# Performance work log

Hardware: AMD Instinct MI355X
Metric: run time of the kernel (lower is better)

The kernel has to match this reference:

```python
import jax, jax.numpy as jnp
import numpy as np

K_SYNAPSES = 32          # numberOfSynapsesPerSegment
THETA = 16               # segment activation threshold (k/2 of the +/-1 synapses)


def _make_weight(key, n_neurons, prev_size, k):
    """Dense int8-style EISANI weight: exactly k synapses per neuron, values +/-1, rest 0.
    Mirrors _initialise_layer_weights (non-EI, dense, static-connection branch)."""
    k1, k2 = jax.random.split(key)
    scores = jax.random.uniform(k1, (n_neurons, prev_size))
    _, idx = jax.lax.top_k(scores, k)  # k distinct random columns per neuron
    signs = jnp.where(jax.random.bernoulli(k2, 0.5, (n_neurons, k)), 1.0, -1.0)
    w = jnp.zeros((n_neurons, prev_size), jnp.float32)
    return w.at[jnp.arange(n_neurons)[:, None], idx].set(signs)


def setup_inputs() -> dict:
    key = jax.random.key(0)
    ks = jax.random.split(key, 5)
    B, F, H, C, L = 1024, 4096, 4096, 10, 3  # batch, encodedFeatureSize, hidden, classes, hidden layers
    # binary encoded tabular input (continuous-var thermometer/gray encoding -> {0,1})
    x = (jax.random.uniform(ks[0], (B, F)) > 0.5).astype(jnp.float32)
    w0 = _make_weight(ks[1], H, F, K_SYNAPSES)
    w1 = _make_weight(ks[2], H, H, K_SYNAPSES)
    w2 = _make_weight(ks[3], H, H, K_SYNAPSES)
    out_conn = jax.random.normal(ks[4], (L, H, C), jnp.float32) * 0.02
    return {"x": x, "w0": w0, "w1": w1, "w2": w2, "out_conn": out_conn}


def reference(x, w0, w1, w2, out_conn):
    # Hidden pass: signed binary connection matmul + threshold activation per layer.
    a = x  # [B, F] in {0,1}
    acts = []
    for w in (w0, w1, w2):
        z = a @ w.T                                   # [B, H] integer-valued dot of {0,1} with {-1,0,+1}
        a = (z >= THETA).astype(jnp.float32)          # segment fires if enough synapses active
        acts.append(a)
    acts = jnp.stack(acts)                            # [L, B, H]
    # Output layer: every hidden layer projects to the class scores.
    return jnp.einsum('lbh,lhc->bc', acts, out_conn)  # [B, C]
```

## Files before the change

### kernel.cpp

```cpp
#include <hip/hip_runtime.h>
#include <stdint.h>


__global__ __launch_bounds__(256) void pack_kernel(const float* __restrict__ x,
                                                   uint64_t* __restrict__ bits) {
    const int c  = blockIdx.x * 256 + threadIdx.x;
    const int bg = blockIdx.y;
    const float* xp = x + (size_t)bg * 64 * 4096 + c;
    uint64_t acc = 0;
#pragma unroll
    for (int r = 0; r < 64; ++r) {
        const float v = xp[(size_t)r * 4096];
        acc |= (uint64_t)(v > 0.5f) << r;
    }
    bits[(size_t)bg * 4096 + c] = acc;
}

__global__ __launch_bounds__(256) void sparsify_kernel(const float* __restrict__ w0,
                                                       const float* __restrict__ w1,
                                                       const float* __restrict__ w2,
                                                       uint32_t* __restrict__ syn) {
    const int wid   = blockIdx.x * 4 + (threadIdx.x >> 6);
    const int lane  = threadIdx.x & 63;
    const int layer = wid >> 12;
    const int r     = wid & 4095;
    const float* wp = (layer == 0 ? w0 : (layer == 1 ? w1 : w2)) + (size_t)r * 4096;
    uint32_t* srow  = syn + (size_t)wid * 32;
    const uint64_t lt = (1ull << lane) - 1ull;
    uint32_t base = 0;
    for (int it = 0; it < 16; ++it) {
        const int col = it * 256 + lane * 4;
        const float4 v = *(const float4*)(wp + col);
        const uint64_t m0 = __ballot(v.x != 0.0f);
        const uint64_t m1 = __ballot(v.y != 0.0f);
        const uint64_t m2 = __ballot(v.z != 0.0f);
        const uint64_t m3 = __ballot(v.w != 0.0f);
        const uint32_t t0 = (uint32_t)__popcll(m0), t1 = (uint32_t)__popcll(m1);
        const uint32_t t2 = (uint32_t)__popcll(m2), t3 = (uint32_t)__popcll(m3);
        if (v.x != 0.0f) { const uint32_t s = base + (uint32_t)__popcll(m0 & lt);
            if (s < 32u) srow[s] = (uint32_t)col | (v.x < 0.0f ? 0x80000000u : 0u); }
        if (v.y != 0.0f) { const uint32_t s = base + t0 + (uint32_t)__popcll(m1 & lt);
            if (s < 32u) srow[s] = (uint32_t)(col + 1) | (v.y < 0.0f ? 0x80000000u : 0u); }
        if (v.z != 0.0f) { const uint32_t s = base + t0 + t1 + (uint32_t)__popcll(m2 & lt);
            if (s < 32u) srow[s] = (uint32_t)(col + 2) | (v.z < 0.0f ? 0x80000000u : 0u); }
        if (v.w != 0.0f) { const uint32_t s = base + t0 + t1 + t2 + (uint32_t)__popcll(m3 & lt);
            if (s < 32u) srow[s] = (uint32_t)(col + 3) | (v.w < 0.0f ? 0x80000000u : 0u); }
        base += t0 + t1 + t2 + t3;
    }
}

__global__ __launch_bounds__(256) void layer_kernel(const uint64_t* __restrict__ in_bits,
                                                    const uint32_t* __restrict__ syn,
                                                    uint64_t* __restrict__ out_bits) {
    __shared__ uint64_t lb[4096];
    const int tid = threadIdx.x;
    const int bg  = blockIdx.y;
    const uint64_t* src = in_bits + (size_t)bg * 4096;
#pragma unroll
    for (int i = 0; i < 8; ++i)
        ((uint4*)lb)[i * 256 + tid] = ((const uint4*)src)[i * 256 + tid];
    __syncthreads();

    const int h = blockIdx.x * 256 + tid;
    const uint32_t* srow = syn + (size_t)h * 32;
    uint32_t sw[32];
#pragma unroll
    for (int k = 0; k < 8; ++k)
        *(uint4*)(sw + k * 4) = *(const uint4*)(srow + k * 4);

    uint32_t thr = 16;
#pragma unroll
    for (int k = 0; k < 32; ++k) thr += sw[k] >> 31;

    uint64_t a0 = 0, a1 = 0, a2 = 0, a3 = 0, a4 = 0;
    uint64_t b0 = 0, b1 = 0, b2 = 0, b3 = 0, b4 = 0;
#pragma unroll
    for (int k = 0; k < 32; k += 2) {
        {
            const uint32_t s = sw[k];
            uint64_t c = lb[s & 4095] ^ (uint64_t)(int64_t)((int32_t)s >> 31);
            uint64_t t;
            t = a0 & c; a0 ^= c; c = t;
            t = a1 & c; a1 ^= c; c = t;
            t = a2 & c; a2 ^= c; c = t;
            t = a3 & c; a3 ^= c; c = t;
            a4 ^= c;
        }
        {
            const uint32_t s = sw[k + 1];
            uint64_t c = lb[s & 4095] ^ (uint64_t)(int64_t)((int32_t)s >> 31);
            uint64_t t;
            t = b0 & c; b0 ^= c; c = t;
            t = b1 & c; b1 ^= c; c = t;
            t = b2 & c; b2 ^= c; c = t;
            t = b3 & c; b3 ^= c; c = t;
            b4 ^= c;
        }
    }
    uint64_t c;
    const uint64_t v0 = a0 ^ b0;     c = a0 & b0;
    const uint64_t v1 = a1 ^ b1 ^ c; c = (a1 & b1) | (c & (a1 ^ b1));
    const uint64_t v2 = a2 ^ b2 ^ c; c = (a2 & b2) | (c & (a2 ^ b2));
    const uint64_t v3 = a3 ^ b3 ^ c; c = (a3 & b3) | (c & (a3 ^ b3));
    const uint64_t v4 = a4 ^ b4 ^ c; c = (a4 & b4) | (c & (a4 ^ b4));
    const uint64_t v5 = c;
    uint64_t gt = 0, eq = ~0ull;
    {
        uint64_t tb;
        tb = ((thr >> 5) & 1u) ? ~0ull : 0ull; gt |= eq & v5 & ~tb; eq &= ~(v5 ^ tb);
        tb = ((thr >> 4) & 1u) ? ~0ull : 0ull; gt |= eq & v4 & ~tb; eq &= ~(v4 ^ tb);
        tb = ((thr >> 3) & 1u) ? ~0ull : 0ull; gt |= eq & v3 & ~tb; eq &= ~(v3 ^ tb);
        tb = ((thr >> 2) & 1u) ? ~0ull : 0ull; gt |= eq & v2 & ~tb; eq &= ~(v2 ^ tb);
        tb = ((thr >> 1) & 1u) ? ~0ull : 0ull; gt |= eq & v1 & ~tb; eq &= ~(v1 ^ tb);
        tb = ((thr >> 0) & 1u) ? ~0ull : 0ull; gt |= eq & v0 & ~tb; eq &= ~(v0 ^ tb);
    }
    out_bits[(size_t)bg * 4096 + h] = gt | eq;
}

__global__ __launch_bounds__(256) void out_kernel(const uint64_t* __restrict__ bits,
                                                  const float* __restrict__ oc,
                                                  float* __restrict__ out) {
    __shared__ float red[4][10];
    const int b   = blockIdx.x;
    const int tid = threadIdx.x;
    const int bg  = b >> 6;
    const int sh  = b & 63;
    float acc[10];
#pragma unroll
    for (int cc = 0; cc < 10; ++cc) acc[cc] = 0.0f;
#pragma unroll
    for (int l = 0; l < 3; ++l) {
        const uint64_t* base = bits + (size_t)l * 65536 + (size_t)bg * 4096;
        const float* ocl = oc + (size_t)l * 40960;
#pragma unroll
        for (int i = 0; i < 16; ++i) {
            const int h = i * 256 + tid;
            const uint64_t w = base[h];
            if ((w >> sh) & 1ull) {
                const float* o = ocl + (size_t)h * 10;
#pragma unroll
                for (int cc = 0; cc < 10; ++cc) acc[cc] += o[cc];
            }
        }
    }
#pragma unroll
    for (int cc = 0; cc < 10; ++cc) {
#pragma unroll
        for (int off = 32; off > 0; off >>= 1) acc[cc] += __shfl_down(acc[cc], off);
    }
    const int wave = tid >> 6;
    if ((tid & 63) == 0) {
#pragma unroll
        for (int cc = 0; cc < 10; ++cc) red[wave][cc] = acc[cc];
    }
    __syncthreads();
    if (tid < 10)
        out[(size_t)b * 10 + tid] = red[0][tid] + red[1][tid] + red[2][tid] + red[3][tid];
}

extern "C" void kernel_launch(void* const* d_in, const int* in_sizes, int n_in,
                              void* d_out, int out_size, void* d_ws, size_t ws_size,
                              hipStream_t stream) {
    const float* x  = (const float*)d_in[0];
    const float* w0 = (const float*)d_in[1];
    const float* w1 = (const float*)d_in[2];
    const float* w2 = (const float*)d_in[3];
    const float* oc = (const float*)d_in[4];
    float* out = (float*)d_out;

    uint32_t* syn   = (uint32_t*)d_ws;
    uint64_t* bitsx = (uint64_t*)((char*)d_ws + 2097152);
    uint64_t* bits0 = bitsx + 65536;
    uint64_t* bits1 = bits0 + 65536;
    uint64_t* bits2 = bits1 + 65536;

    pack_kernel<<<dim3(16, 16), 256, 0, stream>>>(x, bitsx);
    sparsify_kernel<<<3072, 256, 0, stream>>>(w0, w1, w2, syn);

    layer_kernel<<<dim3(16, 16), 256, 0, stream>>>(bitsx, syn,          bits0);
    layer_kernel<<<dim3(16, 16), 256, 0, stream>>>(bits0, syn + 131072, bits1);
    layer_kernel<<<dim3(16, 16), 256, 0, stream>>>(bits1, syn + 262144, bits2);

    out_kernel<<<1024, 256, 0, stream>>>(bits0, oc, out);
}
```

Baseline: 237.0 us.

## Fuse layer and output kernels into one cooperative grid-synced kernel

Merges input packing and weight sparsification into a single prep launch, and batches eight float4 weight loads per wave before the ballot compaction. The three layer passes and the output projection become one cooperative kernel of 256 blocks that calls grid.sync between layers. This removes several launch boundaries and inter-kernel gaps. In exchange, the output stage runs on fewer blocks, and the code now depends on every block being co-resident for the grid barrier.

```diff
diff --git a/kernel.cpp b/kernel.cpp
--- a/kernel.cpp
+++ b/kernel.cpp
@@ -1,161 +1,184 @@
 #include <hip/hip_runtime.h>
+#include <hip/hip_cooperative_groups.h>
 #include <stdint.h>
 
-
-__global__ __launch_bounds__(256) void pack_kernel(const float* __restrict__ x,
+namespace cg = cooperative_groups;
+
+
+__global__ __launch_bounds__(256) void prep_kernel(const float* __restrict__ x,
+                                                   const float* __restrict__ w0,
+                                                   const float* __restrict__ w1,
+                                                   const float* __restrict__ w2,
+                                                   uint32_t* __restrict__ syn,
                                                    uint64_t* __restrict__ bits) {
-    const int c  = blockIdx.x * 256 + threadIdx.x;
-    const int bg = blockIdx.y;
-    const float* xp = x + (size_t)bg * 64 * 4096 + c;
-    uint64_t acc = 0;
-#pragma unroll
-    for (int r = 0; r < 64; ++r) {
-        const float v = xp[(size_t)r * 4096];
-        acc |= (uint64_t)(v > 0.5f) << r;
-    }
-    bits[(size_t)bg * 4096 + c] = acc;
-}
-
-__global__ __launch_bounds__(256) void sparsify_kernel(const float* __restrict__ w0,
-                                                       const float* __restrict__ w1,
-                                                       const float* __restrict__ w2,
-                                                       uint32_t* __restrict__ syn) {
-    const int wid   = blockIdx.x * 4 + (threadIdx.x >> 6);
-    const int lane  = threadIdx.x & 63;
-    const int layer = wid >> 12;
-    const int r     = wid & 4095;
-    const float* wp = (layer == 0 ? w0 : (layer == 1 ? w1 : w2)) + (size_t)r * 4096;
-    uint32_t* srow  = syn + (size_t)wid * 32;
-    const uint64_t lt = (1ull << lane) - 1ull;
-    uint32_t base = 0;
-    for (int it = 0; it < 16; ++it) {
-        const int col = it * 256 + lane * 4;
-        const float4 v = *(const float4*)(wp + col);
-        const uint64_t m0 = __ballot(v.x != 0.0f);
-        const uint64_t m1 = __ballot(v.y != 0.0f);
-        const uint64_t m2 = __ballot(v.z != 0.0f);
-        const uint64_t m3 = __ballot(v.w != 0.0f);
-        const uint32_t t0 = (uint32_t)__popcll(m0), t1 = (uint32_t)__popcll(m1);
-        const uint32_t t2 = (uint32_t)__popcll(m2), t3 = (uint32_t)__popcll(m3);
-        if (v.x != 0.0f) { const uint32_t s = base + (uint32_t)__popcll(m0 & lt);
-            if (s < 32u) srow[s] = (uint32_t)col | (v.x < 0.0f ? 0x80000000u : 0u); }
-        if (v.y != 0.0f) { const uint32_t s = base + t0 + (uint32_t)__popcll(m1 & lt);
-            if (s < 32u) srow[s] = (uint32_t)(col + 1) | (v.y < 0.0f ? 0x80000000u : 0u); }
-        if (v.z != 0.0f) { const uint32_t s = base + t0 + t1 + (uint32_t)__popcll(m2 & lt);
-            if (s < 32u) srow[s] = (uint32_t)(col + 2) | (v.z < 0.0f ? 0x80000000u : 0u); }
-        if (v.w != 0.0f) { const uint32_t s = base + t0 + t1 + t2 + (uint32_t)__popcll(m3 & lt);
-            if (s < 32u) srow[s] = (uint32_t)(col + 3) | (v.w < 0.0f ? 0x80000000u : 0u); }
-        base += t0 + t1 + t2 + t3;
+    const int blk = blockIdx.x;
+    const int tid = threadIdx.x;
+    if (blk < 3072) {
+        const int wid   = blk * 4 + (tid >> 6);
+        const int lane  = tid & 63;
+        const int layer = wid >> 12;
+        const int r     = wid & 4095;
+        const float* wp = (layer == 0 ? w0 : (layer == 1 ? w1 : w2)) + (size_t)r * 4096;
+        const float4* wp4 = (const float4*)wp;
+        uint32_t* srow  = syn + (size_t)wid * 32;
+        const uint64_t lt = (1ull << lane) - 1ull;
+        uint32_t base = 0;
+#pragma unroll
+        for (int half = 0; half < 2; ++half) {
+            float4 v[8];
+#pragma unroll
+            for (int it = 0; it < 8; ++it)
+                v[it] = wp4[half * 512 + it * 64 + lane];
+#pragma unroll
+            for (int it = 0; it < 8; ++it) {
+                const int col = half * 2048 + it * 256 + lane * 4;
+                const float4 q = v[it];
+                const uint64_t m0 = __ballot(q.x != 0.0f);
+                const uint64_t m1 = __ballot(q.y != 0.0f);
+                const uint64_t m2 = __ballot(q.z != 0.0f);
+                const uint64_t m3 = __ballot(q.w != 0.0f);
+                const uint32_t t0 = (uint32_t)__popcll(m0), t1 = (uint32_t)__popcll(m1);
+                const uint32_t t2 = (uint32_t)__popcll(m2), t3 = (uint32_t)__popcll(m3);
+                if (q.x != 0.0f) { const uint32_t s = base + (uint32_t)__popcll(m0 & lt);
+                    if (s < 32u) srow[s] = (uint32_t)col | (q.x < 0.0f ? 0x80000000u : 0u); }
+                if (q.y != 0.0f) { const uint32_t s = base + t0 + (uint32_t)__popcll(m1 & lt);
+                    if (s < 32u) srow[s] = (uint32_t)(col + 1) | (q.y < 0.0f ? 0x80000000u : 0u); }
+                if (q.z != 0.0f) { const uint32_t s = base + t0 + t1 + (uint32_t)__popcll(m2 & lt);
+                    if (s < 32u) srow[s] = (uint32_t)(col + 2) | (q.z < 0.0f ? 0x80000000u : 0u); }
+                if (q.w != 0.0f) { const uint32_t s = base + t0 + t1 + t2 + (uint32_t)__popcll(m3 & lt);
+                    if (s < 32u) srow[s] = (uint32_t)(col + 3) | (q.w < 0.0f ? 0x80000000u : 0u); }
+                base += t0 + t1 + t2 + t3;
+            }
+        }
+    } else {
+        const int blk2 = blk - 3072;
+        const int bg   = blk2 >> 4;
+        const int c    = (blk2 & 15) * 256 + tid;
+        const float* xp = x + (size_t)bg * 64 * 4096 + c;
+        uint64_t acc = 0;
+#pragma unroll
+        for (int rr = 0; rr < 64; ++rr) {
+            const float v = xp[(size_t)rr * 4096];
+            acc |= (uint64_t)(v > 0.5f) << rr;
+        }
+        bits[(size_t)bg * 4096 + c] = acc;
     }
 }
 
-__global__ __launch_bounds__(256) void layer_kernel(const uint64_t* __restrict__ in_bits,
-                                                    const uint32_t* __restrict__ syn,
-                                                    uint64_t* __restrict__ out_bits) {
-    __shared__ uint64_t lb[4096];
-    const int tid = threadIdx.x;
-    const int bg  = blockIdx.y;
-    const uint64_t* src = in_bits + (size_t)bg * 4096;
-#pragma unroll
-    for (int i = 0; i < 8; ++i)
-        ((uint4*)lb)[i * 256 + tid] = ((const uint4*)src)[i * 256 + tid];
-    __syncthreads();
-
-    const int h = blockIdx.x * 256 + tid;
-    const uint32_t* srow = syn + (size_t)h * 32;
-    uint32_t sw[32];
-#pragma unroll
-    for (int k = 0; k < 8; ++k)
-        *(uint4*)(sw + k * 4) = *(const uint4*)(srow + k * 4);
-
-    uint32_t thr = 16;
-#pragma unroll
-    for (int k = 0; k < 32; ++k) thr += sw[k] >> 31;
-
-    uint64_t a0 = 0, a1 = 0, a2 = 0, a3 = 0, a4 = 0;
-    uint64_t b0 = 0, b1 = 0, b2 = 0, b3 = 0, b4 = 0;
-#pragma unroll
-    for (int k = 0; k < 32; k += 2) {
-        {
-            const uint32_t s = sw[k];
-            uint64_t c = lb[s & 4095] ^ (uint64_t)(int64_t)((int32_t)s >> 31);
-            uint64_t t;
-            t = a0 & c; a0 ^= c; c = t;
-            t = a1 & c; a1 ^= c; c = t;
-            t = a2 & c; a2 ^= c; c = t;
-            t = a3 & c; a3 ^= c; c = t;
-            a4 ^= c;
-        }
-        {
-            const uint32_t s = sw[k + 1];
-            uint64_t c = lb[s & 4095] ^ (uint64_t)(int64_t)((int32_t)s >> 31);
-            uint64_t t;
-            t = b0 & c; b0 ^= c; c = t;
-            t = b1 & c; b1 ^= c; c = t;
-            t = b2 & c; b2 ^= c; c = t;
-            t = b3 & c; b3 ^= c; c = t;
-            b4 ^= c;
-        }
-    }
-    uint64_t c;
-    const uint64_t v0 = a0 ^ b0;     c = a0 & b0;
-    const uint64_t v1 = a1 ^ b1 ^ c; c = (a1 & b1) | (c & (a1 ^ b1));
-    const uint64_t v2 = a2 ^ b2 ^ c; c = (a2 & b2) | (c & (a2 ^ b2));
-    const uint64_t v3 = a3 ^ b3 ^ c; c = (a3 & b3) | (c & (a3 ^ b3));
-    const uint64_t v4 = a4 ^ b4 ^ c; c = (a4 & b4) | (c & (a4 ^ b4));
-    const uint64_t v5 = c;
-    uint64_t gt = 0, eq = ~0ull;
-    {
-        uint64_t tb;
-        tb = ((thr >> 5) & 1u) ? ~0ull : 0ull; gt |= eq & v5 & ~tb; eq &= ~(v5 ^ tb);
-        tb = ((thr >> 4) & 1u) ? ~0ull : 0ull; gt |= eq & v4 & ~tb; eq &= ~(v4 ^ tb);
-        tb = ((thr >> 3) & 1u) ? ~0ull : 0ull; gt |= eq & v3 & ~tb; eq &= ~(v3 ^ tb);
-        tb = ((thr >> 2) & 1u) ? ~0ull : 0ull; gt |= eq & v2 & ~tb; eq &= ~(v2 ^ tb);
-        tb = ((thr >> 1) & 1u) ? ~0ull : 0ull; gt |= eq & v1 & ~tb; eq &= ~(v1 ^ tb);
-        tb = ((thr >> 0) & 1u) ? ~0ull : 0ull; gt |= eq & v0 & ~tb; eq &= ~(v0 ^ tb);
-    }
-    out_bits[(size_t)bg * 4096 + h] = gt | eq;
-}
-
-__global__ __launch_bounds__(256) void out_kernel(const uint64_t* __restrict__ bits,
+__global__ __launch_bounds__(256) void net_kernel(const uint64_t* __restrict__ bitsx,
+                                                  const uint32_t* __restrict__ syn,
+                                                  uint64_t* __restrict__ bits,
                                                   const float* __restrict__ oc,
                                                   float* __restrict__ out) {
+    __shared__ uint64_t lb[4096];
     __shared__ float red[4][10];
-    const int b   = blockIdx.x;
-    const int tid = threadIdx.x;
-    const int bg  = b >> 6;
-    const int sh  = b & 63;
-    float acc[10];
-#pragma unroll
-    for (int cc = 0; cc < 10; ++cc) acc[cc] = 0.0f;
-#pragma unroll
+    const int tid  = threadIdx.x;
+    const int blk  = blockIdx.x;
+    const int bg   = blk >> 4;
+    const int hblk = blk & 15;
+    cg::grid_group grid = cg::this_grid();
+
     for (int l = 0; l < 3; ++l) {
-        const uint64_t* base = bits + (size_t)l * 65536 + (size_t)bg * 4096;
-        const float* ocl = oc + (size_t)l * 40960;
-#pragma unroll
-        for (int i = 0; i < 16; ++i) {
-            const int h = i * 256 + tid;
-            const uint64_t w = base[h];
-            if ((w >> sh) & 1ull) {
-                const float* o = ocl + (size_t)h * 10;
-#pragma unroll
-                for (int cc = 0; cc < 10; ++cc) acc[cc] += o[cc];
-            }
-        }
+        const uint64_t* in = (l == 0) ? bitsx : (bits + (size_t)(l - 1) * 65536);
+        const uint64_t* src = in + (size_t)bg * 4096;
+#pragma unroll
+        for (int i = 0; i < 8; ++i)
+            ((uint4*)lb)[i * 256 + tid] = ((const uint4*)src)[i * 256 + tid];
+        __syncthreads();
+
+        const int h = hblk * 256 + tid;
+        const uint32_t* srow = syn + (size_t)l * 131072 + (size_t)h * 32;
+        uint32_t sw[32];
+#pragma unroll
+        for (int k = 0; k < 8; ++k)
+            *(uint4*)(sw + k * 4) = *(const uint4*)(srow + k * 4);
+
+        uint32_t thr = 16;
+#pragma unroll
+        for (int k = 0; k < 32; ++k) thr += sw[k] >> 31;
+
+        uint64_t a0 = 0, a1 = 0, a2 = 0, a3 = 0, a4 = 0;
+        uint64_t b0 = 0, b1 = 0, b2 = 0, b3 = 0, b4 = 0;
+#pragma unroll
+        for (int k = 0; k < 32; k += 2) {
+            {
+                const uint32_t s = sw[k];
+                uint64_t c = lb[s & 4095] ^ (uint64_t)(int64_t)((int32_t)s >> 31);
+                uint64_t t;
+                t = a0 & c; a0 ^= c; c = t;
+                t = a1 & c; a1 ^= c; c = t;
+                t = a2 & c; a2 ^= c; c = t;
+                t = a3 & c; a3 ^= c; c = t;
+                a4 ^= c;
+            }
+            {
+                const uint32_t s = sw[k + 1];
+                uint64_t c = lb[s & 4095] ^ (uint64_t)(int64_t)((int32_t)s >> 31);
+                uint64_t t;
+                t = b0 & c; b0 ^= c; c = t;
+                t = b1 & c; b1 ^= c; c = t;
+                t = b2 & c; b2 ^= c; c = t;
+                t = b3 & c; b3 ^= c; c = t;
+                b4 ^= c;
+            }
+        }
+        uint64_t c;
+        const uint64_t v0 = a0 ^ b0;     c = a0 & b0;
+        const uint64_t v1 = a1 ^ b1 ^ c; c = (a1 & b1) | (c & (a1 ^ b1));
+        const uint64_t v2 = a2 ^ b2 ^ c; c = (a2 & b2) | (c & (a2 ^ b2));
+        const uint64_t v3 = a3 ^ b3 ^ c; c = (a3 & b3) | (c & (a3 ^ b3));
+        const uint64_t v4 = a4 ^ b4 ^ c; c = (a4 & b4) | (c & (a4 ^ b4));
+        const uint64_t v5 = c;
+        uint64_t gt = 0, eq = ~0ull;
+        {
+            uint64_t tb;
+            tb = ((thr >> 5) & 1u) ? ~0ull : 0ull; gt |= eq & v5 & ~tb; eq &= ~(v5 ^ tb);
+            tb = ((thr >> 4) & 1u) ? ~0ull : 0ull; gt |= eq & v4 & ~tb; eq &= ~(v4 ^ tb);
+            tb = ((thr >> 3) & 1u) ? ~0ull : 0ull; gt |= eq & v3 & ~tb; eq &= ~(v3 ^ tb);
+            tb = ((thr >> 2) & 1u) ? ~0ull : 0ull; gt |= eq & v2 & ~tb; eq &= ~(v2 ^ tb);
+            tb = ((thr >> 1) & 1u) ? ~0ull : 0ull; gt |= eq & v1 & ~tb; eq &= ~(v1 ^ tb);
+            tb = ((thr >> 0) & 1u) ? ~0ull : 0ull; gt |= eq & v0 & ~tb; eq &= ~(v0 ^ tb);
+        }
+        (bits + (size_t)l * 65536)[(size_t)bg * 4096 + h] = gt | eq;
+        grid.sync();
     }
-#pragma unroll
-    for (int cc = 0; cc < 10; ++cc) {
-#pragma unroll
-        for (int off = 32; off > 0; off >>= 1) acc[cc] += __shfl_down(acc[cc], off);
+
+    for (int rep = 0; rep < 4; ++rep) {
+        const int b   = rep * 256 + blk;
+        const int obg = b >> 6;
+        const int sh  = b & 63;
+        float acc[10];
+#pragma unroll
+        for (int cc = 0; cc < 10; ++cc) acc[cc] = 0.0f;
+#pragma unroll
+        for (int l = 0; l < 3; ++l) {
+            const uint64_t* base = bits + (size_t)l * 65536 + (size_t)obg * 4096;
+            const float* ocl = oc + (size_t)l * 40960;
+#pragma unroll
+            for (int i = 0; i < 16; ++i) {
+                const int h = i * 256 + tid;
+                if ((base[h] >> sh) & 1ull) {
+                    const float* o = ocl + (size_t)h * 10;
+#pragma unroll
+                    for (int cc = 0; cc < 10; ++cc) acc[cc] += o[cc];
+                }
+            }
+        }
+#pragma unroll
+        for (int cc = 0; cc < 10; ++cc) {
+#pragma unroll
+            for (int off = 32; off > 0; off >>= 1) acc[cc] += __shfl_down(acc[cc], off);
+        }
+        const int wave = tid >> 6;
+        if ((tid & 63) == 0) {
+#pragma unroll
+            for (int cc = 0; cc < 10; ++cc) red[wave][cc] = acc[cc];
+        }
+        __syncthreads();
+        if (tid < 10)
+            out[(size_t)b * 10 + tid] = red[0][tid] + red[1][tid] + red[2][tid] + red[3][tid];
+        __syncthreads();
     }
-    const int wave = tid >> 6;
-    if ((tid & 63) == 0) {
-#pragma unroll
-        for (int cc = 0; cc < 10; ++cc) red[wave][cc] = acc[cc];
-    }
-    __syncthreads();
-    if (tid < 10)
-        out[(size_t)b * 10 + tid] = red[0][tid] + red[1][tid] + red[2][tid] + red[3][tid];
 }
 
 extern "C" void kernel_launch(void* const* d_in, const int* in_sizes, int n_in,
@@ -171,15 +194,12 @@
     uint32_t* syn   = (uint32_t*)d_ws;
     uint64_t* bitsx = (uint64_t*)((char*)d_ws + 2097152);
     uint64_t* bits0 = bitsx + 65536;
-    uint64_t* bits1 = bits0 + 65536;
-    uint64_t* bits2 = bits1 + 65536;
-
-    pack_kernel<<<dim3(16, 16), 256, 0, stream>>>(x, bitsx);
-    sparsify_kernel<<<3072, 256, 0, stream>>>(w0, w1, w2, syn);
-
-    layer_kernel<<<dim3(16, 16), 256, 0, stream>>>(bitsx, syn,          bits0);
-    layer_kernel<<<dim3(16, 16), 256, 0, stream>>>(bits0, syn + 131072, bits1);
-    layer_kernel<<<dim3(16, 16), 256, 0, stream>>>(bits1, syn + 262144, bits2);
-
-    out_kernel<<<1024, 256, 0, stream>>>(bits0, oc, out);
+
+    prep_kernel<<<3328, 256, 0, stream>>>(x, w0, w1, w2, syn, bitsx);
+
+    const uint64_t* bitsx_c = bitsx;
+    const uint32_t* syn_c   = syn;
+    void* args[] = {(void*)&bitsx_c, (void*)&syn_c, (void*)&bits0, (void*)&oc, (void*)&out};
+    hipLaunchCooperativeKernel((const void*)net_kernel, dim3(256), dim3(256),
+                               args, 0, stream);
 }
```

Result: slower. 361.9 us (+52.7%).

## Restructure output projection into split-K partials, batch sparsify loads

Applied to the files above, without the earlier changes.

The output layer is reorganised so that each wave handles 64 hidden rows for 64 batch rows. Each lane uses its bit as a float multiplier against a shared out_conn row, so every weight row is read once and reused across 64 samples instead of once per sample. A second small kernel reduces the 48 partial chunks per batch group. The sparsify kernel now issues four float4 loads at once before the ballots to increase memory-level parallelism, and its launch order is swapped with pack. The partial buffer reuses the synapse workspace region, which is safe only because the layer kernels have already consumed it.

```diff
diff --git a/kernel.cpp b/kernel.cpp
--- a/kernel.cpp
+++ b/kernel.cpp
@@ -1,20 +1,6 @@
 #include <hip/hip_runtime.h>
 #include <stdint.h>
 
-
-__global__ __launch_bounds__(256) void pack_kernel(const float* __restrict__ x,
-                                                   uint64_t* __restrict__ bits) {
-    const int c  = blockIdx.x * 256 + threadIdx.x;
-    const int bg = blockIdx.y;
-    const float* xp = x + (size_t)bg * 64 * 4096 + c;
-    uint64_t acc = 0;
-#pragma unroll
-    for (int r = 0; r < 64; ++r) {
-        const float v = xp[(size_t)r * 4096];
-        acc |= (uint64_t)(v > 0.5f) << r;
-    }
-    bits[(size_t)bg * 4096 + c] = acc;
-}
 
 __global__ __launch_bounds__(256) void sparsify_kernel(const float* __restrict__ w0,
                                                        const float* __restrict__ w1,
@@ -25,28 +11,50 @@
     const int layer = wid >> 12;
     const int r     = wid & 4095;
     const float* wp = (layer == 0 ? w0 : (layer == 1 ? w1 : w2)) + (size_t)r * 4096;
+    const float4* wp4 = (const float4*)wp;
     uint32_t* srow  = syn + (size_t)wid * 32;
     const uint64_t lt = (1ull << lane) - 1ull;
     uint32_t base = 0;
-    for (int it = 0; it < 16; ++it) {
-        const int col = it * 256 + lane * 4;
-        const float4 v = *(const float4*)(wp + col);
-        const uint64_t m0 = __ballot(v.x != 0.0f);
-        const uint64_t m1 = __ballot(v.y != 0.0f);
-        const uint64_t m2 = __ballot(v.z != 0.0f);
-        const uint64_t m3 = __ballot(v.w != 0.0f);
-        const uint32_t t0 = (uint32_t)__popcll(m0), t1 = (uint32_t)__popcll(m1);
-        const uint32_t t2 = (uint32_t)__popcll(m2), t3 = (uint32_t)__popcll(m3);
-        if (v.x != 0.0f) { const uint32_t s = base + (uint32_t)__popcll(m0 & lt);
-            if (s < 32u) srow[s] = (uint32_t)col | (v.x < 0.0f ? 0x80000000u : 0u); }
-        if (v.y != 0.0f) { const uint32_t s = base + t0 + (uint32_t)__popcll(m1 & lt);
-            if (s < 32u) srow[s] = (uint32_t)(col + 1) | (v.y < 0.0f ? 0x80000000u : 0u); }
-        if (v.z != 0.0f) { const uint32_t s = base + t0 + t1 + (uint32_t)__popcll(m2 & lt);
-            if (s < 32u) srow[s] = (uint32_t)(col + 2) | (v.z < 0.0f ? 0x80000000u : 0u); }
-        if (v.w != 0.0f) { const uint32_t s = base + t0 + t1 + t2 + (uint32_t)__popcll(m3 & lt);
-            if (s < 32u) srow[s] = (uint32_t)(col + 3) | (v.w < 0.0f ? 0x80000000u : 0u); }
-        base += t0 + t1 + t2 + t3;
-    }
+    for (int grp = 0; grp < 4; ++grp) {
+        float4 v[4];
+#pragma unroll
+        for (int it = 0; it < 4; ++it)
+            v[it] = wp4[grp * 256 + it * 64 + lane];
+#pragma unroll
+        for (int it = 0; it < 4; ++it) {
+            const int col = grp * 1024 + it * 256 + lane * 4;
+            const float4 q = v[it];
+            const uint64_t m0 = __ballot(q.x != 0.0f);
+            const uint64_t m1 = __ballot(q.y != 0.0f);
+            const uint64_t m2 = __ballot(q.z != 0.0f);
+            const uint64_t m3 = __ballot(q.w != 0.0f);
+            const uint32_t t0 = (uint32_t)__popcll(m0), t1 = (uint32_t)__popcll(m1);
+            const uint32_t t2 = (uint32_t)__popcll(m2), t3 = (uint32_t)__popcll(m3);
+            if (q.x != 0.0f) { const uint32_t s = base + (uint32_t)__popcll(m0 & lt);
+                if (s < 32u) srow[s] = (uint32_t)col | (q.x < 0.0f ? 0x80000000u : 0u); }
+            if (q.y != 0.0f) { const uint32_t s = base + t0 + (uint32_t)__popcll(m1 & lt);
+                if (s < 32u) srow[s] = (uint32_t)(col + 1) | (q.y < 0.0f ? 0x80000000u : 0u); }
+            if (q.z != 0.0f) { const uint32_t s = base + t0 + t1 + (uint32_t)__popcll(m2 & lt);
+                if (s < 32u) srow[s] = (uint32_t)(col + 2) | (q.z < 0.0f ? 0x80000000u : 0u); }
+            if (q.w != 0.0f) { const uint32_t s = base + t0 + t1 + t2 + (uint32_t)__popcll(m3 & lt);
+                if (s < 32u) srow[s] = (uint32_t)(col + 3) | (q.w < 0.0f ? 0x80000000u : 0u); }
+            base += t0 + t1 + t2 + t3;
+        }
+    }
+}
+
+__global__ __launch_bounds__(256) void pack_kernel(const float* __restrict__ x,
+                                                   uint64_t* __restrict__ bits) {
+    const int c  = blockIdx.x * 256 + threadIdx.x;
+    const int bg = blockIdx.y;
+    const float* xp = x + (size_t)bg * 64 * 4096 + c;
+    uint64_t acc = 0;
+#pragma unroll
+    for (int r = 0; r < 64; ++r) {
+        const float v = xp[(size_t)r * 4096];
+        acc |= (uint64_t)(v > 0.5f) << r;
+    }
+    bits[(size_t)bg * 4096 + c] = acc;
 }
 
 __global__ __launch_bounds__(256) void layer_kernel(const uint64_t* __restrict__ in_bits,
@@ -117,45 +125,56 @@
     out_bits[(size_t)bg * 4096 + h] = gt | eq;
 }
 
-__global__ __launch_bounds__(256) void out_kernel(const uint64_t* __restrict__ bits,
-                                                  const float* __restrict__ oc,
-                                                  float* __restrict__ out) {
-    __shared__ float red[4][10];
-    const int b   = blockIdx.x;
-    const int tid = threadIdx.x;
-    const int bg  = b >> 6;
-    const int sh  = b & 63;
+__global__ __launch_bounds__(256) void outA_kernel(const uint64_t* __restrict__ bits,
+                                                   const float* __restrict__ oc,
+                                                   float* __restrict__ partial) {
+    __shared__ float red[4][640];
+    const int tid   = threadIdx.x;
+    const int chunk = blockIdx.x;
+    const int bg    = blockIdx.y;
+    const int wave  = tid >> 6;
+    const int lane  = tid & 63;
+    const int r0 = chunk * 256 + wave * 64;
+    const int l  = r0 >> 12;
+    const int h0 = r0 & 4095;
+    const uint64_t* bw = bits + (size_t)l * 65536 + (size_t)bg * 4096 + h0;
+    const float* op = oc + (size_t)r0 * 10;
+
     float acc[10];
 #pragma unroll
     for (int cc = 0; cc < 10; ++cc) acc[cc] = 0.0f;
-#pragma unroll
-    for (int l = 0; l < 3; ++l) {
-        const uint64_t* base = bits + (size_t)l * 65536 + (size_t)bg * 4096;
-        const float* ocl = oc + (size_t)l * 40960;
-#pragma unroll
-        for (int i = 0; i < 16; ++i) {
-            const int h = i * 256 + tid;
-            const uint64_t w = base[h];
-            if ((w >> sh) & 1ull) {
-                const float* o = ocl + (size_t)h * 10;
-#pragma unroll
-                for (int cc = 0; cc < 10; ++cc) acc[cc] += o[cc];
-            }
-        }
-    }
-#pragma unroll
-    for (int cc = 0; cc < 10; ++cc) {
-#pragma unroll
-        for (int off = 32; off > 0; off >>= 1) acc[cc] += __shfl_down(acc[cc], off);
-    }
-    const int wave = tid >> 6;
-    if ((tid & 63) == 0) {
-#pragma unroll
-        for (int cc = 0; cc < 10; ++cc) red[wave][cc] = acc[cc];
-    }
+
+#pragma unroll 4
+    for (int i = 0; i < 64; ++i) {
+        const uint64_t w = bw[i];
+        const float bitf = (float)((w >> lane) & 1ull);
+        const float2* o2 = (const float2*)(op + (size_t)i * 10);
+        const float2 p0 = o2[0], p1 = o2[1], p2 = o2[2], p3 = o2[3], p4 = o2[4];
+        acc[0] += bitf * p0.x; acc[1] += bitf * p0.y;
+        acc[2] += bitf * p1.x; acc[3] += bitf * p1.y;
+        acc[4] += bitf * p2.x; acc[5] += bitf * p2.y;
+        acc[6] += bitf * p3.x; acc[7] += bitf * p3.y;
+        acc[8] += bitf * p4.x; acc[9] += bitf * p4.y;
+    }
+#pragma unroll
+    for (int cc = 0; cc < 10; ++cc) red[wave][lane * 10 + cc] = acc[cc];
     __syncthreads();
-    if (tid < 10)
-        out[(size_t)b * 10 + tid] = red[0][tid] + red[1][tid] + red[2][tid] + red[3][tid];
+
+    float* dst = partial + ((size_t)bg * 48 + chunk) * 640;
+    for (int idx = tid; idx < 640; idx += 256)
+        dst[idx] = red[0][idx] + red[1][idx] + red[2][idx] + red[3][idx];
+}
+
+__global__ __launch_bounds__(256) void outB_kernel(const float* __restrict__ partial,
+                                                   float* __restrict__ out) {
+    const int g  = blockIdx.x * 256 + threadIdx.x;
+    const int bg = g / 640;
+    const int s  = g - bg * 640;
+    const float* p = partial + (size_t)bg * 48 * 640 + s;
+    float sum = 0.0f;
+#pragma unroll
+    for (int ch = 0; ch < 48; ++ch) sum += p[ch * 640];
+    out[g] = sum;
 }
 
 extern "C" void kernel_launch(void* const* d_in, const int* in_sizes, int n_in,
@@ -168,18 +187,20 @@
     const float* oc = (const float*)d_in[4];
     float* out = (float*)d_out;
 
-    uint32_t* syn   = (uint32_t*)d_ws;
-    uint64_t* bitsx = (uint64_t*)((char*)d_ws + 2097152);
-    uint64_t* bits0 = bitsx + 65536;
-    uint64_t* bits1 = bits0 + 65536;
-    uint64_t* bits2 = bits1 + 65536;
-
+    uint32_t* syn    = (uint32_t*)d_ws;
+    float*    part   = (float*)d_ws;
+    uint64_t* bitsx  = (uint64_t*)((char*)d_ws + 2097152);
+    uint64_t* bits0  = bitsx + 65536;
+    uint64_t* bits1  = bits0 + 65536;
+    uint64_t* bits2  = bits1 + 65536;
+
+    sparsify_kernel<<<3072, 256, 0, stream>>>(w0, w1, w2, syn);
     pack_kernel<<<dim3(16, 16), 256, 0, stream>>>(x, bitsx);
-    sparsify_kernel<<<3072, 256, 0, stream>>>(w0, w1, w2, syn);
 
     layer_kernel<<<dim3(16, 16), 256, 0, stream>>>(bitsx, syn,          bits0);
     layer_kernel<<<dim3(16, 16), 256, 0, stream>>>(bits0, syn + 131072, bits1);
     layer_kernel<<<dim3(16, 16), 256, 0, stream>>>(bits1, syn + 262144, bits2);
 
-    out_kernel<<<1024, 256, 0, stream>>>(bits0, oc, out);
-}
+    outA_kernel<<<dim3(48, 16), 256, 0, stream>>>(bits0, oc, part);
+    outB_kernel<<<40, 256, 0, stream>>>(part, out);
+}
```

Measured after the change: 250.3 us. 1.06x slower.
